# Kernel optimization log

Hardware: AMD Instinct MI355X
Metric: run time of the kernel (lower is better)

## Reference

```python
import jax, jax.numpy as jnp
import numpy as np

N, E, G = 20000, 100000, 32
HID, HEADS, HC = 64, 8, 64  # hidden, heads, per-head channels (PyG: out_channels per head)
L, K = 3, 4


def setup_inputs() -> dict:
    key = jax.random.key(0)
    ks = jax.random.split(key, 20)
    rn = lambda k, s, sc=0.05: jax.random.normal(k, s, jnp.float32) * sc
    HO = HEADS * HC  # 512
    return {
        "x": jax.random.uniform(ks[0], (N, 7), jnp.float32),
        "edge_attr": jax.random.normal(ks[1], (E, 4), jnp.float32),
        "means": jax.random.normal(ks[2], (K, 8), jnp.float32),
        "log_stds": jnp.zeros((K, 8), jnp.float32),
        "sp_W": rn(ks[3], (K, HID), 0.3), "sp_b": jnp.zeros((HID,), jnp.float32),
        "ne_W": rn(ks[4], (7, HID), 0.3), "ne_b": jnp.zeros((HID,), jnp.float32),
        "ee_W": rn(ks[5], (4, HID), 0.3), "ee_b": jnp.zeros((HID,), jnp.float32),
        "Wq": rn(ks[6], (L, HID, HO)), "bq": jnp.zeros((L, HO), jnp.float32),
        "Wk": rn(ks[7], (L, HID, HO)), "bk": jnp.zeros((L, HO), jnp.float32),
        "Wv": rn(ks[8], (L, HID, HO)), "bv": jnp.zeros((L, HO), jnp.float32),
        "We": rn(ks[9], (L, HID, HO)), "be": jnp.zeros((L, HO), jnp.float32),
        "Ws": rn(ks[10], (L, HID, HID)), "bs": jnp.zeros((L, HID), jnp.float32),
        "eu_W": rn(ks[11], (L, 3 * HID, HID)), "eu_b": jnp.zeros((L, HID), jnp.float32),
        "rW1": rn(ks[12], (2 * HID, HID)), "rb1": jnp.zeros((HID,), jnp.float32),
        "rW2": rn(ks[13], (HID, HID)), "rb2": jnp.zeros((HID,), jnp.float32),
        "rW3": rn(ks[14], (HID, 2)), "rb3": jnp.zeros((2,), jnp.float32),
        "edge_index": jax.random.randint(ks[15], (2, E), 0, N, jnp.int32),
        "batch": jnp.sort(jax.random.randint(ks[16], (N,), 0, G, jnp.int32)),
        "num_graphs": G,
    }


def reference(x, edge_attr, means, log_stds, sp_W, sp_b, ne_W, ne_b, ee_W, ee_b,
              Wq, bq, Wk, bk, Wv, bv, We, be, Ws, bs, eu_W, eu_b,
              rW1, rb1, rW2, rb2, rW3, rb3, edge_index, batch, num_graphs):
    n = x.shape[0]
    src, dst = edge_index[0], edge_index[1]

    # ---- SpatialGaussianEncoder (dropout is identity in eval) ----
    p = x[:, :4]
    sl, sr = p[src, :2], p[src, 2:4]
    dl, dr = p[dst, :2], p[dst, 2:4]
    rel = jnp.stack([dl - sl, dl - sr, dr - sl, dr - sr], axis=1)  # [E,4,2]
    dist = jnp.linalg.norm(rel, axis=-1)                           # [E,4]
    ang = jnp.arctan2(rel[..., 1], rel[..., 0])                    # [E,4]
    u = jnp.stack([dist, ang], axis=-1).reshape(-1, 8)             # [E,8] (d,a)x4
    std = jnp.exp(log_stds) + 1e-6                                 # [K,8]
    z = (u[:, None, :] - means[None]) / std[None]                  # [E,K,8]
    w = jnp.exp(-0.5 * jnp.sum(z * z, axis=-1))                    # [E,K]
    sp = jax.nn.relu(w @ sp_W + sp_b)                              # [E,HID]

    h = jax.nn.relu(x @ ne_W + ne_b)                               # [N,HID]
    ea = jax.nn.relu(edge_attr @ ee_W + ee_b) + sp                 # [E,HID]

    scale = 1.0 / float(np.sqrt(HC))
    for l in range(L):
        # PyG TransformerConv(hidden, hidden, heads=8, edge_dim=hidden, concat=False)
        q = (h @ Wq[l] + bq[l]).reshape(n, HEADS, HC)
        k = (h @ Wk[l] + bk[l]).reshape(n, HEADS, HC)
        v = (h @ Wv[l] + bv[l]).reshape(n, HEADS, HC)
        e = (ea @ We[l] + be[l]).reshape(-1, HEADS, HC)
        kj = k[src] + e                                            # [E,H,C]
        alpha = jnp.einsum('ehc,ehc->eh', q[dst], kj) * scale      # [E,H]
        m = jax.ops.segment_max(alpha, dst, num_segments=n)
        ex = jnp.exp(alpha - m[dst])
        den = jax.ops.segment_sum(ex, dst, num_segments=n)
        a = ex / (den[dst] + 1e-16)                                # scatter-softmax over dst
        msg = a[:, :, None] * (v[src] + e)                         # [E,H,C]
        out = jax.ops.segment_sum(msg, dst, num_segments=n).mean(axis=1)  # concat=False -> head mean
        h = jax.nn.relu(out + h @ Ws[l] + bs[l])                   # skip (root_weight) + F.relu
        ef = jnp.concatenate([h[src], h[dst], ea], axis=1)         # [E,3*HID]
        ea = jax.nn.relu(ef @ eu_W[l] + eu_b[l])

    # ---- per-graph masked-mean pooling == segment mean ----
    cn = jnp.maximum(jax.ops.segment_sum(jnp.ones((n,), x.dtype), batch, num_segments=num_graphs), 1.0)
    node_pool = jax.ops.segment_sum(h, batch, num_segments=num_graphs) / cn[:, None]
    eb = batch[src]
    ce = jnp.maximum(jax.ops.segment_sum(jnp.ones((src.shape[0],), x.dtype), eb, num_segments=num_graphs), 1.0)
    edge_pool = jax.ops.segment_sum(ea, eb, num_segments=num_graphs) / ce[:, None]
    g = jnp.concatenate([node_pool, edge_pool], axis=1)            # [G,2*HID]

    h1 = jax.nn.relu(g @ rW1 + rb1)
    h2 = jax.nn.relu(h1 @ rW2 + rb2)
    return jnp.tanh(h2 @ rW3 + rb3)                                # [G,2]
```

## Files before the change

### kernel.cpp

```cpp
#include <hip/hip_runtime.h>
#include <hip/hip_bf16.h>
#include <cstdint>
#include <cstddef>



__global__ void __launch_bounds__(256) k_node_embed(
    const float* __restrict__ x, const float* __restrict__ neW, const float* __restrict__ neb,
    float* __restrict__ h, int N)
{
    int idx = blockIdx.x * 256 + threadIdx.x;
    int n = idx >> 6, c = idx & 63;
    if (n >= N) return;
    float acc = neb[c];
    #pragma unroll
    for (int j = 0; j < 7; ++j) acc += x[(size_t)n * 7 + j] * neW[j * 64 + c];
    h[(size_t)n * 64 + c] = fmaxf(acc, 0.f);
}

__global__ void __launch_bounds__(256) k_edge_w(
    const float* __restrict__ x,
    const float* __restrict__ means, const float* __restrict__ log_stds,
    const int2* __restrict__ ipair, const int* __restrict__ idst,
    float* __restrict__ wbuf, int E)
{
    int slot = blockIdx.x * 256 + threadIdx.x;
    if (slot >= E) return;
    int s = ipair[slot].x, d = idst[slot];
    const float* ps = x + (size_t)s * 7;
    const float* pd = x + (size_t)d * 7;
    float slx = ps[0], sly = ps[1], srx = ps[2], sry = ps[3];
    float dlx = pd[0], dly = pd[1], drx = pd[2], dry = pd[3];
    float u[8];
    float rx, ry;
    rx = dlx - slx; ry = dly - sly; u[0] = sqrtf(rx*rx + ry*ry); u[1] = atan2f(ry, rx);
    rx = dlx - srx; ry = dly - sry; u[2] = sqrtf(rx*rx + ry*ry); u[3] = atan2f(ry, rx);
    rx = drx - slx; ry = dry - sly; u[4] = sqrtf(rx*rx + ry*ry); u[5] = atan2f(ry, rx);
    rx = drx - srx; ry = dry - sry; u[6] = sqrtf(rx*rx + ry*ry); u[7] = atan2f(ry, rx);
    #pragma unroll
    for (int kk = 0; kk < 4; ++kk) {
        float ssum = 0.f;
        #pragma unroll
        for (int dd = 0; dd < 8; ++dd) {
            float stdv = expf(log_stds[kk*8+dd]) + 1e-6f;
            float z = (u[dd] - means[kk*8+dd]) / stdv;
            ssum += z * z;
        }
        wbuf[(size_t)slot*4 + kk] = expf(-0.5f * ssum);
    }
}

__global__ void __launch_bounds__(256) k_edge_ea(
    const float* __restrict__ edge_attr, const float* __restrict__ wbuf,
    const int2* __restrict__ ipair,
    const float* __restrict__ spW, const float* __restrict__ spb,
    const float* __restrict__ eeW, const float* __restrict__ eeb,
    float* __restrict__ ea, int E)
{
    int idx = blockIdx.x * 256 + threadIdx.x;
    int slot = idx >> 6, c = idx & 63;
    if (slot >= E) return;
    int e = ipair[slot].y;
    float acce = eeb[c];
    #pragma unroll
    for (int j = 0; j < 4; ++j) acce += edge_attr[(size_t)e*4 + j] * eeW[j*64 + c];
    float accs = spb[c];
    #pragma unroll
    for (int j = 0; j < 4; ++j) accs += wbuf[(size_t)slot*4 + j] * spW[j*64 + c];
    ea[(size_t)slot*64 + c] = fmaxf(acce, 0.f) + fmaxf(accs, 0.f);
}


__global__ void __launch_bounds__(256) k_hist(
    const int* __restrict__ dst, int* __restrict__ deg, int E)
{
    int e = blockIdx.x * 256 + threadIdx.x;
    if (e < E) atomicAdd(deg + dst[e], 1);
}

__global__ void __launch_bounds__(1024) k_scan(
    const int* __restrict__ deg, int* __restrict__ ptr, int* __restrict__ headw, int N)
{
    __shared__ int part[1024];
    int t = threadIdx.x;
    int per = (N + 1023) / 1024;
    int s = 0;
    for (int i = 0; i < per; ++i) { int idx = t*per + i; if (idx < N) s += deg[idx]; }
    part[t] = s;
    __syncthreads();
    for (int off = 1; off < 1024; off <<= 1) {
        int v = (t >= off) ? part[t - off] : 0;
        __syncthreads();
        part[t] += v;
        __syncthreads();
    }
    int base = (t > 0) ? part[t - 1] : 0;
    for (int i = 0; i < per; ++i) {
        int idx = t*per + i;
        if (idx < N) { ptr[idx] = base; headw[idx] = base; base += deg[idx]; }
    }
    if (t == 1023) ptr[N] = part[1023];
}

__global__ void __launch_bounds__(256) k_scatter(
    const int* __restrict__ dst, const int* __restrict__ src, const int* __restrict__ batch,
    int* __restrict__ headw, int2* __restrict__ ipair, int* __restrict__ idst,
    int* __restrict__ iebs, int E)
{
    int e = blockIdx.x * 256 + threadIdx.x;
    if (e < E) {
        int s = src[e];
        int d = dst[e];
        int pos = atomicAdd(headw + d, 1);
        ipair[pos] = make_int2(s, e);
        idst[pos] = d;
        iebs[pos] = batch[s];
    }
}


__global__ void __launch_bounds__(256) k_wprod_all(
    const float* __restrict__ Wq, const float* __restrict__ bq,
    const float* __restrict__ Wk, const float* __restrict__ We,
    float* __restrict__ Mk, float* __restrict__ Me,
    float* __restrict__ bqk, float* __restrict__ bqe)
{
    int h = blockIdx.x;
    int which = blockIdx.y;
    int l = blockIdx.z;
    const float* Wq_l = Wq + (size_t)l * 64 * 512;
    const float* bq_l = bq + (size_t)l * 512;
    const float* Wx_l = (which ? We : Wk) + (size_t)l * 64 * 512;
    float* M  = (which ? Me : Mk) + (size_t)l * 64 * 512;
    float* bM = (which ? bqe : bqk) + (size_t)l * 512;
    __shared__ float wq_s[65][64];
    __shared__ float wx_s[64][65];
    int tid = threadIdx.x;
    for (int i = tid; i < 4096; i += 256) {
        int r = i >> 6, c2 = i & 63;
        wq_s[r][c2] = Wq_l[(size_t)r*512 + h*64 + c2];
        wx_s[r][c2] = Wx_l[(size_t)r*512 + h*64 + c2];
    }
    if (tid < 64) wq_s[64][tid] = bq_l[h*64 + tid];
    __syncthreads();
    int j = tid & 63, cg = tid >> 6;
    for (int c = cg*16; c < cg*16 + 16; ++c) {
        float s = 0.f;
        #pragma unroll 8
        for (int c2 = 0; c2 < 64; ++c2) s += wq_s[c][c2] * wx_s[j][c2];
        M[(size_t)c*512 + h*64 + j] = s;
    }
    if (tid < 64) {
        float s = 0.f;
        #pragma unroll 8
        for (int c2 = 0; c2 < 64; ++c2) s += wq_s[64][c2] * wx_s[tid][c2];
        bM[h*64 + tid] = s;
    }
}

__global__ void __launch_bounds__(64) k_wqb_all(
    const float* __restrict__ Wq, const float* __restrict__ bq,
    const float* __restrict__ bk, const float* __restrict__ be,
    float* __restrict__ wqb, float* __restrict__ cb)
{
    int l = blockIdx.x;
    const float* Wq_l = Wq + (size_t)l * 64 * 512;
    const float* bq_l = bq + (size_t)l * 512;
    const float* bk_l = bk + (size_t)l * 512;
    const float* be_l = be + (size_t)l * 512;
    float* wqb_l = wqb + (size_t)l * 512;
    float* cb_l  = cb + (size_t)l * 8;
    int c = threadIdx.x;
    for (int h = 0; h < 8; ++h) {
        float s = 0.f;
        for (int c2 = 0; c2 < 64; ++c2)
            s += Wq_l[(size_t)c*512 + h*64 + c2] * (bk_l[h*64+c2] + be_l[h*64+c2]);
        wqb_l[c*8 + h] = s;
    }
    if (c < 8) {
        float s = 0.f;
        for (int c2 = 0; c2 < 64; ++c2)
            s += bq_l[c*64 + c2] * (bk_l[c*64+c2] + be_l[c*64+c2]);
        cb_l[c] = s;
    }
}


__global__ void __launch_bounds__(256) k_proj16(
    const float* __restrict__ h,
    const float* __restrict__ Mk, const float* __restrict__ bqk, float* __restrict__ qk,
    const float* __restrict__ Me, const float* __restrict__ bqe, float* __restrict__ qe2,
    int N)
{
    __shared__ float As[64][132];
    __shared__ __align__(16) float Wt[64][64];
    int tid = threadIdx.x;
    int y = blockIdx.y;
    int which = y >> 3, yb = y & 7;
    const float* W    = which ? Me : Mk;
    const float* bias = (which ? bqe : bqk) + yb * 64;
    float* Y          = which ? qe2 : qk;
    int n0 = blockIdx.x * 128;
    {
        int rt = tid & 127;
        int n = n0 + rt;
        int jh = (tid >> 7) * 32;
        if (n < N) {
            const float* ap = h + (size_t)n*64;
            #pragma unroll
            for (int j4 = 0; j4 < 8; ++j4) {
                int j = jh + j4 * 4;
                float4 a = *(const float4*)(ap + j);
                As[j+0][rt] = a.x; As[j+1][rt] = a.y;
                As[j+2][rt] = a.z; As[j+3][rt] = a.w;
            }
        } else {
            #pragma unroll
            for (int j4 = 0; j4 < 8; ++j4) {
                int j = jh + j4 * 4;
                As[j+0][rt] = 0.f; As[j+1][rt] = 0.f;
                As[j+2][rt] = 0.f; As[j+3][rt] = 0.f;
            }
        }
        #pragma unroll
        for (int i = 0; i < 4; ++i) {
            int idx = tid + i * 256;
            int j = idx >> 4, c4 = (idx & 15) * 4;
            *(float4*)&Wt[j][c4] = *(const float4*)(W + (size_t)j*512 + yb*64 + c4);
        }
    }
    __syncthreads();
    int wv = tid >> 6, lane = tid & 63;
    int rg = lane >> 3, cg = lane & 7;
    int c0 = cg * 8;
    int rbase = wv * 32 + rg * 4;
    float acc[4][8];
    float4 b0 = *(const float4*)(bias + c0);
    float4 b1 = *(const float4*)(bias + c0 + 4);
    #pragma unroll
    for (int t = 0; t < 4; ++t) {
        acc[t][0]=b0.x; acc[t][1]=b0.y; acc[t][2]=b0.z; acc[t][3]=b0.w;
        acc[t][4]=b1.x; acc[t][5]=b1.y; acc[t][6]=b1.z; acc[t][7]=b1.w;
    }
    #pragma unroll 4
    for (int j = 0; j < 64; ++j) {
        float4 av = *(const float4*)&As[j][rbase];
        float4 w0 = *(const float4*)&Wt[j][c0];
        float4 w1 = *(const float4*)&Wt[j][c0 + 4];
        acc[0][0] += av.x*w0.x; acc[0][1] += av.x*w0.y; acc[0][2] += av.x*w0.z; acc[0][3] += av.x*w0.w;
        acc[0][4] += av.x*w1.x; acc[0][5] += av.x*w1.y; acc[0][6] += av.x*w1.z; acc[0][7] += av.x*w1.w;
        acc[1][0] += av.y*w0.x; acc[1][1] += av.y*w0.y; acc[1][2] += av.y*w0.z; acc[1][3] += av.y*w0.w;
        acc[1][4] += av.y*w1.x; acc[1][5] += av.y*w1.y; acc[1][6] += av.y*w1.z; acc[1][7] += av.y*w1.w;
        acc[2][0] += av.z*w0.x; acc[2][1] += av.z*w0.y; acc[2][2] += av.z*w0.z; acc[2][3] += av.z*w0.w;
        acc[2][4] += av.z*w1.x; acc[2][5] += av.z*w1.y; acc[2][6] += av.z*w1.z; acc[2][7] += av.z*w1.w;
        acc[3][0] += av.w*w0.x; acc[3][1] += av.w*w0.y; acc[3][2] += av.w*w0.z; acc[3][3] += av.w*w0.w;
        acc[3][4] += av.w*w1.x; acc[3][5] += av.w*w1.y; acc[3][6] += av.w*w1.z; acc[3][7] += av.w*w1.w;
    }
    #pragma unroll
    for (int t = 0; t < 4; ++t) {
        int n = n0 + rbase + t;
        if (n < N) {
            float4 o0 = {acc[t][0],acc[t][1],acc[t][2],acc[t][3]};
            float4 o1 = {acc[t][4],acc[t][5],acc[t][6],acc[t][7]};
            *(float4*)(Y + (size_t)n*512 + yb*64 + c0)     = o0;
            *(float4*)(Y + (size_t)n*512 + yb*64 + c0 + 4) = o1;
        }
    }
}


__global__ void __launch_bounds__(256) k_attn_fused(
    const float* __restrict__ qk, const float* __restrict__ qe2,
    const float* __restrict__ wqb, const float* __restrict__ cb,
    const float* __restrict__ ea, const float* __restrict__ hbuf,
    const int* __restrict__ ptr, const int2* __restrict__ ipair,
    float* __restrict__ hagg, float* __restrict__ tbuf, float* __restrict__ sbuf, int N)
{
    int wv = threadIdx.x >> 6, lane = threadIdx.x & 63;
    int n = blockIdx.x * 4 + wv;
    if (n >= N) return;
    int h = lane >> 3, p = lane & 7;
    int b = ptr[n], e_ = ptr[n + 1];
    int deg = e_ - b;
    const float4* xp = (const float4*)(qk + (size_t)n*512 + lane*8);
    float4 x0 = xp[0], x1 = xp[1];
    const float4* gp = (const float4*)(qe2 + (size_t)n*512 + lane*8);
    float4 g0 = gp[0], g1 = gp[1];
    const float4* hdp = (const float4*)(hbuf + (size_t)n*64 + p*8);
    float4 hd0 = hdp[0], hd1 = hdp[1];
    float qbh = hd0.x*wqb[(p*8+0)*8+h] + hd0.y*wqb[(p*8+1)*8+h]
              + hd0.z*wqb[(p*8+2)*8+h] + hd0.w*wqb[(p*8+3)*8+h]
              + hd1.x*wqb[(p*8+4)*8+h] + hd1.y*wqb[(p*8+5)*8+h]
              + hd1.z*wqb[(p*8+6)*8+h] + hd1.w*wqb[(p*8+7)*8+h];
    qbh += __shfl_xor(qbh, 1);
    qbh += __shfl_xor(qbh, 2);
    qbh += __shfl_xor(qbh, 4);
    qbh += cb[h];
    float m = -3.4e38f, den = 0.f;
    float hacc[8], tacc[8];
    #pragma unroll
    for (int i = 0; i < 8; ++i) { hacc[i] = 0.f; tacc[i] = 0.f; }
    for (int base = 0; base < deg; base += 64) {
        int cnt = deg - base; if (cnt > 64) cnt = 64;
        int2 myp = (lane < cnt) ? ipair[b + base + lane] : make_int2(0, 0);
        int s0i = __shfl(myp.x, 0);
        const float4* hp = (const float4*)(hbuf + (size_t)s0i*64 + p*8);
        const float4* ap = (const float4*)(ea + (size_t)(b + base)*64 + p*8);
        float4 h0 = hp[0], h1 = hp[1];
        float4 a0 = ap[0], a1 = ap[1];
        for (int i = 0; i < cnt; ++i) {
            float4 h0c = h0, h1c = h1, a0c = a0, a1c = a1;
            if (i + 1 < cnt) {
                int sn = __shfl(myp.x, i + 1);
                const float4* hpn = (const float4*)(hbuf + (size_t)sn*64 + p*8);
                const float4* apn = (const float4*)(ea + (size_t)(b + base + i + 1)*64 + p*8);
                h0 = hpn[0]; h1 = hpn[1]; a0 = apn[0]; a1 = apn[1];
            }
            float t = x0.x*h0c.x + x0.y*h0c.y + x0.z*h0c.z + x0.w*h0c.w
                    + x1.x*h1c.x + x1.y*h1c.y + x1.z*h1c.z + x1.w*h1c.w
                    + g0.x*a0c.x + g0.y*a0c.y + g0.z*a0c.z + g0.w*a0c.w
                    + g1.x*a1c.x + g1.y*a1c.y + g1.z*a1c.z + g1.w*a1c.w;
            t += __shfl_xor(t, 1);
            t += __shfl_xor(t, 2);
            t += __shfl_xor(t, 4);
            float al = 0.125f * (t + qbh);
            float mn = fmaxf(m, al);
            float r = expf(m - mn);
            float w = expf(al - mn);
            den = den * r + w;
            m = mn;
            hacc[0] = hacc[0]*r + w*h0c.x; hacc[1] = hacc[1]*r + w*h0c.y;
            hacc[2] = hacc[2]*r + w*h0c.z; hacc[3] = hacc[3]*r + w*h0c.w;
            hacc[4] = hacc[4]*r + w*h1c.x; hacc[5] = hacc[5]*r + w*h1c.y;
            hacc[6] = hacc[6]*r + w*h1c.z; hacc[7] = hacc[7]*r + w*h1c.w;
            tacc[0] = tacc[0]*r + w*a0c.x; tacc[1] = tacc[1]*r + w*a0c.y;
            tacc[2] = tacc[2]*r + w*a0c.z; tacc[3] = tacc[3]*r + w*a0c.w;
            tacc[4] = tacc[4]*r + w*a1c.x; tacc[5] = tacc[5]*r + w*a1c.y;
            tacc[6] = tacc[6]*r + w*a1c.z; tacc[7] = tacc[7]*r + w*a1c.w;
        }
    }
    float inv = 0.125f / (den + 1e-16f);
    float4 o;
    o = {hacc[0]*inv,hacc[1]*inv,hacc[2]*inv,hacc[3]*inv};
    *(float4*)(hagg + (size_t)n*512 + lane*8)     = o;
    o = {hacc[4]*inv,hacc[5]*inv,hacc[6]*inv,hacc[7]*inv};
    *(float4*)(hagg + (size_t)n*512 + lane*8 + 4) = o;
    o = {tacc[0]*inv,tacc[1]*inv,tacc[2]*inv,tacc[3]*inv};
    *(float4*)(tbuf + (size_t)n*512 + lane*8)     = o;
    o = {tacc[4]*inv,tacc[5]*inv,tacc[6]*inv,tacc[7]*inv};
    *(float4*)(tbuf + (size_t)n*512 + lane*8 + 4) = o;
    if (p == 0) sbuf[(size_t)n*8 + h] = den * inv;
}

__global__ void __launch_bounds__(256) k_nf_gemm2(
    const float* __restrict__ tbuf, const float* __restrict__ hagg,
    const float* __restrict__ We, const float* __restrict__ Wv,
    float* __restrict__ pbuf, int N)
{
    __shared__ float As[64][132];
    __shared__ __align__(16) float Wt[64][64];
    int tid = threadIdx.x;
    int y = blockIdx.y;
    int n0 = blockIdx.x * 128;
    int wv = tid >> 6, lane = tid & 63;
    int rg = lane >> 3, cg = lane & 7;
    int c0 = cg * 8;
    int rbase = wv * 32 + rg * 4;
    float acc[4][8];
    #pragma unroll
    for (int t = 0; t < 4; ++t)
        #pragma unroll
        for (int i = 0; i < 8; ++i) acc[t][i] = 0.f;
    #pragma unroll
    for (int round = 0; round < 2; ++round) {
        const float* A = round ? hagg : tbuf;
        const float* W = round ? Wv : We;
        if (round) __syncthreads();
        {
            int rt = tid & 127;
            int n = n0 + rt;
            int jh = (tid >> 7) * 32;
            if (n < N) {
                const float* ap = A + (size_t)n*512 + y*64;
                #pragma unroll
                for (int j4 = 0; j4 < 8; ++j4) {
                    int j = jh + j4 * 4;
                    float4 a = *(const float4*)(ap + j);
                    As[j+0][rt] = a.x; As[j+1][rt] = a.y;
                    As[j+2][rt] = a.z; As[j+3][rt] = a.w;
                }
            } else {
                #pragma unroll
                for (int j4 = 0; j4 < 8; ++j4) {
                    int j = jh + j4 * 4;
                    As[j+0][rt] = 0.f; As[j+1][rt] = 0.f;
                    As[j+2][rt] = 0.f; As[j+3][rt] = 0.f;
                }
            }
            #pragma unroll
            for (int i = 0; i < 4; ++i) {
                int idx = tid + i * 256;
                int j = idx >> 4, c4 = (idx & 15) * 4;
                *(float4*)&Wt[j][c4] = *(const float4*)(W + (size_t)j*512 + y*64 + c4);
            }
        }
        __syncthreads();
        #pragma unroll 4
        for (int j = 0; j < 64; ++j) {
            float4 av = *(const float4*)&As[j][rbase];
            float4 w0 = *(const float4*)&Wt[j][c0];
            float4 w1 = *(const float4*)&Wt[j][c0 + 4];
            acc[0][0] += av.x*w0.x; acc[0][1] += av.x*w0.y; acc[0][2] += av.x*w0.z; acc[0][3] += av.x*w0.w;
            acc[0][4] += av.x*w1.x; acc[0][5] += av.x*w1.y; acc[0][6] += av.x*w1.z; acc[0][7] += av.x*w1.w;
            acc[1][0] += av.y*w0.x; acc[1][1] += av.y*w0.y; acc[1][2] += av.y*w0.z; acc[1][3] += av.y*w0.w;
            acc[1][4] += av.y*w1.x; acc[1][5] += av.y*w1.y; acc[1][6] += av.y*w1.z; acc[1][7] += av.y*w1.w;
            acc[2][0] += av.z*w0.x; acc[2][1] += av.z*w0.y; acc[2][2] += av.z*w0.z; acc[2][3] += av.z*w0.w;
            acc[2][4] += av.z*w1.x; acc[2][5] += av.z*w1.y; acc[2][6] += av.z*w1.z; acc[2][7] += av.z*w1.w;
            acc[3][0] += av.w*w0.x; acc[3][1] += av.w*w0.y; acc[3][2] += av.w*w0.z; acc[3][3] += av.w*w0.w;
            acc[3][4] += av.w*w1.x; acc[3][5] += av.w*w1.y; acc[3][6] += av.w*w1.z; acc[3][7] += av.w*w1.w;
        }
    }
    float* out = pbuf + (size_t)y * N * 64;
    #pragma unroll
    for (int t = 0; t < 4; ++t) {
        int n = n0 + rbase + t;
        if (n < N) {
            float4 o0 = {acc[t][0],acc[t][1],acc[t][2],acc[t][3]};
            float4 o1 = {acc[t][4],acc[t][5],acc[t][6],acc[t][7]};
            *(float4*)(out + (size_t)n*64 + c0)     = o0;
            *(float4*)(out + (size_t)n*64 + c0 + 4) = o1;
        }
    }
}

__global__ void __launch_bounds__(256) k_nf_reduce2(
    const float* __restrict__ pbuf, const float* __restrict__ hin,
    const float* __restrict__ sbuf, const float* __restrict__ Ws,
    const float* __restrict__ be, const float* __restrict__ bv,
    const float* __restrict__ bs, float* __restrict__ hnext, int N)
{
    int idx = blockIdx.x * 256 + threadIdx.x;
    int n = idx >> 6, cc = idx & 63;
    if (n >= N) return;
    float a = bs[cc];
    #pragma unroll
    for (int y = 0; y < 8; ++y) a += pbuf[(size_t)y*N*64 + (size_t)n*64 + cc];
    float hv = hin[(size_t)n*64 + cc];
    #pragma unroll 8
    for (int j = 0; j < 64; ++j) a += __shfl(hv, j) * Ws[(size_t)j*64 + cc];
    #pragma unroll
    for (int h = 0; h < 8; ++h)
        a += sbuf[(size_t)n*8 + h] * (be[h*64 + cc] + bv[h*64 + cc]);
    hnext[(size_t)n*64 + cc] = fmaxf(a, 0.f);
}

__global__ void __launch_bounds__(256) k_eu_pre(
    const float* __restrict__ h, const float* __restrict__ euW,
    float* __restrict__ hw, int N)
{
    __shared__ float As[64][132];
    __shared__ __align__(16) float Wt[64][64];
    int tid = threadIdx.x;
    int y = blockIdx.y;
    int n0 = blockIdx.x * 128;
    {
        int rt = tid & 127;
        int n = n0 + rt;
        int jh = (tid >> 7) * 32;
        if (n < N) {
            const float* ap = h + (size_t)n*64;
            #pragma unroll
            for (int j4 = 0; j4 < 8; ++j4) {
                int j = jh + j4 * 4;
                float4 a = *(const float4*)(ap + j);
                As[j+0][rt] = a.x; As[j+1][rt] = a.y;
                As[j+2][rt] = a.z; As[j+3][rt] = a.w;
            }
        } else {
            #pragma unroll
            for (int j4 = 0; j4 < 8; ++j4) {
                int j = jh + j4 * 4;
                As[j+0][rt] = 0.f; As[j+1][rt] = 0.f;
                As[j+2][rt] = 0.f; As[j+3][rt] = 0.f;
            }
        }
        #pragma unroll
        for (int i = 0; i < 4; ++i) {
            int idx = tid + i * 256;
            *(float4*)&Wt[idx >> 4][(idx & 15) * 4] =
                *(const float4*)(euW + (size_t)y*4096 + idx * 4);
        }
    }
    __syncthreads();
    int wv = tid >> 6, lane = tid & 63;
    int rg = lane >> 3, cg = lane & 7;
    int c0 = cg * 8;
    int rbase = wv * 32 + rg * 4;
    float acc[4][8];
    #pragma unroll
    for (int t = 0; t < 4; ++t)
        #pragma unroll
        for (int i = 0; i < 8; ++i) acc[t][i] = 0.f;
    #pragma unroll 4
    for (int j = 0; j < 64; ++j) {
        float4 av = *(const float4*)&As[j][rbase];
        float4 w0 = *(const float4*)&Wt[j][c0];
        float4 w1 = *(const float4*)&Wt[j][c0 + 4];
        acc[0][0] += av.x*w0.x; acc[0][1] += av.x*w0.y; acc[0][2] += av.x*w0.z; acc[0][3] += av.x*w0.w;
        acc[0][4] += av.x*w1.x; acc[0][5] += av.x*w1.y; acc[0][6] += av.x*w1.z; acc[0][7] += av.x*w1.w;
        acc[1][0] += av.y*w0.x; acc[1][1] += av.y*w0.y; acc[1][2] += av.y*w0.z; acc[1][3] += av.y*w0.w;
        acc[1][4] += av.y*w1.x; acc[1][5] += av.y*w1.y; acc[1][6] += av.y*w1.z; acc[1][7] += av.y*w1.w;
        acc[2][0] += av.z*w0.x; acc[2][1] += av.z*w0.y; acc[2][2] += av.z*w0.z; acc[2][3] += av.z*w0.w;
        acc[2][4] += av.z*w1.x; acc[2][5] += av.z*w1.y; acc[2][6] += av.z*w1.z; acc[2][7] += av.z*w1.w;
        acc[3][0] += av.w*w0.x; acc[3][1] += av.w*w0.y; acc[3][2] += av.w*w0.z; acc[3][3] += av.w*w0.w;
        acc[3][4] += av.w*w1.x; acc[3][5] += av.w*w1.y; acc[3][6] += av.w*w1.z; acc[3][7] += av.w*w1.w;
    }
    #pragma unroll
    for (int t = 0; t < 4; ++t) {
        int n = n0 + rbase + t;
        if (n < N) {
            float4 o0 = {acc[t][0],acc[t][1],acc[t][2],acc[t][3]};
            float4 o1 = {acc[t][4],acc[t][5],acc[t][6],acc[t][7]};
            *(float4*)(hw + (size_t)n*128 + y*64 + c0)     = o0;
            *(float4*)(hw + (size_t)n*128 + y*64 + c0 + 4) = o1;
        }
    }
}

__global__ void __launch_bounds__(256) k_edge_update2(
    const float* __restrict__ hw, const float* __restrict__ ea,
    const float* __restrict__ euW2, const float* __restrict__ eub,
    const int2* __restrict__ ipair, const int* __restrict__ idst,
    float* __restrict__ ea2, int E)
{
    __shared__ float As[64][132];
    __shared__ __align__(16) float Wt[64][64];
    __shared__ int sid[128], did[128];
    int tid = threadIdx.x;
    int e0 = blockIdx.x * 128;
    if (tid < 128) {
        int slot = e0 + tid; if (slot >= E) slot = E - 1;
        sid[tid] = ipair[slot].x; did[tid] = idst[slot];
    }
    {
        int et = tid & 127;
        int slot = e0 + et; if (slot >= E) slot = E - 1;
        const float* ap = ea + (size_t)slot * 64;
        int jh = (tid >> 7) * 32;
        #pragma unroll
        for (int j4 = 0; j4 < 8; ++j4) {
            int j = jh + j4 * 4;
            float4 a = *(const float4*)(ap + j);
            As[j+0][et] = a.x; As[j+1][et] = a.y;
            As[j+2][et] = a.z; As[j+3][et] = a.w;
        }
        #pragma unroll
        for (int i = 0; i < 4; ++i) {
            int idx = tid + i * 256;
            *(float4*)&Wt[idx >> 4][(idx & 15) * 4] = *(const float4*)(euW2 + idx * 4);
        }
    }
    __syncthreads();
    int wv = tid >> 6, lane = tid & 63;
    int rg = lane >> 3, cg = lane & 7;
    int c0 = cg * 8;
    int rbase = wv * 32 + rg * 4;
    float acc[4][8];
    float4 b0 = *(const float4*)(eub + c0);
    float4 b1 = *(const float4*)(eub + c0 + 4);
    #pragma unroll
    for (int t = 0; t < 4; ++t) {
        acc[t][0]=b0.x; acc[t][1]=b0.y; acc[t][2]=b0.z; acc[t][3]=b0.w;
        acc[t][4]=b1.x; acc[t][5]=b1.y; acc[t][6]=b1.z; acc[t][7]=b1.w;
    }
    #pragma unroll 4
    for (int j = 0; j < 64; ++j) {
        float4 av = *(const float4*)&As[j][rbase];
        float4 w0 = *(const float4*)&Wt[j][c0];
        float4 w1 = *(const float4*)&Wt[j][c0 + 4];
        acc[0][0] += av.x*w0.x; acc[0][1] += av.x*w0.y; acc[0][2] += av.x*w0.z; acc[0][3] += av.x*w0.w;
        acc[0][4] += av.x*w1.x; acc[0][5] += av.x*w1.y; acc[0][6] += av.x*w1.z; acc[0][7] += av.x*w1.w;
        acc[1][0] += av.y*w0.x; acc[1][1] += av.y*w0.y; acc[1][2] += av.y*w0.z; acc[1][3] += av.y*w0.w;
        acc[1][4] += av.y*w1.x; acc[1][5] += av.y*w1.y; acc[1][6] += av.y*w1.z; acc[1][7] += av.y*w1.w;
        acc[2][0] += av.z*w0.x; acc[2][1] += av.z*w0.y; acc[2][2] += av.z*w0.z; acc[2][3] += av.z*w0.w;
        acc[2][4] += av.z*w1.x; acc[2][5] += av.z*w1.y; acc[2][6] += av.z*w1.z; acc[2][7] += av.z*w1.w;
        acc[3][0] += av.w*w0.x; acc[3][1] += av.w*w0.y; acc[3][2] += av.w*w0.z; acc[3][3] += av.w*w0.w;
        acc[3][4] += av.w*w1.x; acc[3][5] += av.w*w1.y; acc[3][6] += av.w*w1.z; acc[3][7] += av.w*w1.w;
    }
    #pragma unroll
    for (int t = 0; t < 4; ++t) {
        int slot = e0 + rbase + t;
        if (slot < E) {
            int s = sid[rbase + t], d = did[rbase + t];
            const float4* sp = (const float4*)(hw + (size_t)s*128 + c0);
            const float4* dp = (const float4*)(hw + (size_t)d*128 + 64 + c0);
            float4 s0 = sp[0], s1 = sp[1];
            float4 d0 = dp[0], d1 = dp[1];
            float4 o0 = {fmaxf(acc[t][0]+s0.x+d0.x,0.f), fmaxf(acc[t][1]+s0.y+d0.y,0.f),
                         fmaxf(acc[t][2]+s0.z+d0.z,0.f), fmaxf(acc[t][3]+s0.w+d0.w,0.f)};
            float4 o1 = {fmaxf(acc[t][4]+s1.x+d1.x,0.f), fmaxf(acc[t][5]+s1.y+d1.y,0.f),
                         fmaxf(acc[t][6]+s1.z+d1.z,0.f), fmaxf(acc[t][7]+s1.w+d1.w,0.f)};
            *(float4*)(ea2 + (size_t)slot*64 + c0)     = o0;
            *(float4*)(ea2 + (size_t)slot*64 + c0 + 4) = o1;
        }
    }
}


__global__ void __launch_bounds__(64) k_node_pool(
    const float* __restrict__ h, const int* __restrict__ batch,
    float* __restrict__ npool, float* __restrict__ cn, int N)
{
    int lane = threadIdx.x;
    int n0 = blockIdx.x * 64;
    float acc = 0.f; int cur = -1; int run = 0;
    for (int i = 0; i < 64; ++i) {
        int n = n0 + i;
        if (n >= N) break;
        int b = batch[n];
        if (b != cur) {
            if (cur >= 0) {
                atomicAdd(npool + (size_t)cur*64 + lane, acc);
                if (lane == 0) atomicAdd(cn + cur, (float)run);
            }
            cur = b; acc = 0.f; run = 0;
        }
        acc += h[(size_t)n*64 + lane];
        ++run;
    }
    if (cur >= 0) {
        atomicAdd(npool + (size_t)cur*64 + lane, acc);
        if (lane == 0) atomicAdd(cn + cur, (float)run);
    }
}

__global__ void __launch_bounds__(256) k_edge_pool2(
    const float* __restrict__ ea, const int* __restrict__ iebs,
    float* __restrict__ rep, int E)
{
    __shared__ float pool_s[32][64];
    __shared__ float cnt_s[32];
    int tid = threadIdx.x;
    for (int i = tid; i < 2048; i += 256) ((float*)pool_s)[i] = 0.f;
    if (tid < 32) cnt_s[tid] = 0.f;
    __syncthreads();
    int wv = tid >> 6, lane = tid & 63;
    int base = blockIdx.x * 64 + wv * 16;
    int b16[16]; float v16[16];
    #pragma unroll
    for (int u = 0; u < 16; ++u) {
        int slot = base + u;
        bool ok = (slot < E);
        b16[u] = ok ? iebs[slot] : -1;
        v16[u] = ok ? ea[(size_t)slot*64 + lane] : 0.f;
    }
    #pragma unroll
    for (int u = 0; u < 16; ++u) {
        if (b16[u] >= 0) {
            atomicAdd(&pool_s[b16[u]][lane], v16[u]);
            if (lane == 0) atomicAdd(&cnt_s[b16[u]], 1.f);
        }
    }
    __syncthreads();
    float* myrep = rep + (size_t)(blockIdx.x & 7) * 2080;
    for (int i = tid; i < 2048; i += 256) atomicAdd(myrep + i, ((float*)pool_s)[i]);
    if (tid < 32) atomicAdd(myrep + 2048 + tid, cnt_s[tid]);
}

__global__ void __launch_bounds__(256) k_pool_merge(
    const float* __restrict__ rep, float* __restrict__ epool, float* __restrict__ ce)
{
    int i = blockIdx.x * 256 + threadIdx.x;
    if (i < 2080) {
        float s = 0.f;
        #pragma unroll
        for (int r = 0; r < 8; ++r) s += rep[(size_t)r*2080 + i];
        if (i < 2048) epool[i] = s; else ce[i - 2048] = s;
    }
}

__global__ void __launch_bounds__(64) k_head_mlp(
    const float* __restrict__ npool, const float* __restrict__ epool,
    const float* __restrict__ cn, const float* __restrict__ ce,
    const float* __restrict__ rW1, const float* __restrict__ rb1,
    const float* __restrict__ rW2, const float* __restrict__ rb2,
    const float* __restrict__ rW3, const float* __restrict__ rb3,
    float* __restrict__ out)
{
    __shared__ float g[128];
    __shared__ float h1[64];
    __shared__ float h2[64];
    int b = blockIdx.x, lane = threadIdx.x;
    float cnv = fmaxf(cn[b], 1.f), cev = fmaxf(ce[b], 1.f);
    g[lane]      = npool[(size_t)b*64 + lane] / cnv;
    g[64 + lane] = epool[(size_t)b*64 + lane] / cev;
    __syncthreads();
    float acc = rb1[lane];
    #pragma unroll 4
    for (int j = 0; j < 128; ++j) acc += g[j] * rW1[j*64 + lane];
    h1[lane] = fmaxf(acc, 0.f);
    __syncthreads();
    acc = rb2[lane];
    #pragma unroll 4
    for (int j = 0; j < 64; ++j) acc += h1[j] * rW2[j*64 + lane];
    h2[lane] = fmaxf(acc, 0.f);
    __syncthreads();
    if (lane < 2) {
        float o = rb3[lane];
        for (int j = 0; j < 64; ++j) o += h2[j] * rW3[j*2 + lane];
        out[b*2 + lane] = tanhf(o);
    }
}


extern "C" void kernel_launch(void* const* d_in, const int* in_sizes, int n_in,
                              void* d_out, int out_size, void* d_ws, size_t ws_size,
                              hipStream_t stream)
{
    const float* x         = (const float*)d_in[0];
    const float* edge_attr = (const float*)d_in[1];
    const float* means     = (const float*)d_in[2];
    const float* log_stds  = (const float*)d_in[3];
    const float* spW       = (const float*)d_in[4];
    const float* spb       = (const float*)d_in[5];
    const float* neW       = (const float*)d_in[6];
    const float* neb       = (const float*)d_in[7];
    const float* eeW       = (const float*)d_in[8];
    const float* eeb       = (const float*)d_in[9];
    const float* Wq        = (const float*)d_in[10];
    const float* bq        = (const float*)d_in[11];
    const float* Wk        = (const float*)d_in[12];
    const float* bk        = (const float*)d_in[13];
    const float* Wv        = (const float*)d_in[14];
    const float* bv        = (const float*)d_in[15];
    const float* We        = (const float*)d_in[16];
    const float* be        = (const float*)d_in[17];
    const float* Ws        = (const float*)d_in[18];
    const float* bs        = (const float*)d_in[19];
    const float* euW       = (const float*)d_in[20];
    const float* eub       = (const float*)d_in[21];
    const float* rW1       = (const float*)d_in[22];
    const float* rb1       = (const float*)d_in[23];
    const float* rW2       = (const float*)d_in[24];
    const float* rb2       = (const float*)d_in[25];
    const float* rW3       = (const float*)d_in[26];
    const float* rb3       = (const float*)d_in[27];
    const int* eidx        = (const int*)d_in[28];
    const int* batch       = (const int*)d_in[29];

    int N = in_sizes[0] / 7;
    int E = in_sizes[1] / 4;
    const int G = 32;
    const int* srcp = eidx;
    const int* dstp = eidx + E;

    float* ws = (float*)d_ws;
    size_t fl = 0;
    float* hA    = ws + fl; fl += (size_t)N * 64;
    float* hB    = ws + fl; fl += (size_t)N * 64;
    float* eaA   = ws + fl; fl += (size_t)E * 64;
    float* eaB   = ws + fl; fl += (size_t)E * 64;
    float* B1    = ws + fl; fl += (size_t)N * 512;
    float* B2    = ws + fl; fl += (size_t)N * 512;
    float* B3    = ws + fl; fl += (size_t)N * 512;
    float* alpha = ws + fl; fl += (size_t)E * 8;
    float* sbuf  = ws + fl; fl += (size_t)N * 8;
    float* npool = ws + fl; fl += (size_t)G * 64;
    float* epool = ws + fl; fl += (size_t)G * 64;
    float* cn    = ws + fl; fl += G;
    float* ce    = ws + fl; fl += G;
    float* Mk3   = ws + fl; fl += 3 * 64 * 512;
    float* Me3   = ws + fl; fl += 3 * 64 * 512;
    float* bqk3  = ws + fl; fl += 3 * 512;
    float* bqe3  = ws + fl; fl += 3 * 512;
    float* wqb3  = ws + fl; fl += 3 * 512;
    float* cb3   = ws + fl; fl += 24;
    float* rep   = ws + fl; fl += 8 * 2080;
    int* ideg  = (int*)(ws + fl); fl += (size_t)N;
    int* ihead = (int*)(ws + fl); fl += (size_t)N;
    int2* ipair = (int2*)(ws + fl); fl += (size_t)E * 2;
    int* idst  = (int*)(ws + fl); fl += (size_t)E;
    int* iebs  = (int*)(ws + fl); fl += (size_t)E;
    int* iptr  = (int*)(ws + fl); fl += (size_t)N + 1;

    float* wbuf = alpha;

    hipMemsetAsync(npool, 0, (size_t)(G * 130) * sizeof(float), stream);
    hipMemsetAsync(rep, 0, (size_t)(8 * 2080) * sizeof(float), stream);
    hipMemsetAsync(ideg, 0, (size_t)N * sizeof(int), stream);

    k_node_embed<<<(N * 64 + 255) / 256, 256, 0, stream>>>(x, neW, neb, hA, N);
    k_hist<<<(E + 255) / 256, 256, 0, stream>>>(dstp, ideg, E);
    k_scan<<<1, 1024, 0, stream>>>(ideg, iptr, ihead, N);
    k_scatter<<<(E + 255) / 256, 256, 0, stream>>>(dstp, srcp, batch, ihead,
                                                   ipair, idst, iebs, E);
    k_edge_w<<<(E + 255) / 256, 256, 0, stream>>>(x, means, log_stds, ipair, idst, wbuf, E);
    k_edge_ea<<<((size_t)E * 64 + 255) / 256, 256, 0, stream>>>(edge_attr, wbuf, ipair,
                                                                spW, spb, eeW, eeb, eaA, E);
    k_wprod_all<<<dim3(8, 2, 3), 256, 0, stream>>>(Wq, bq, Wk, We, Mk3, Me3, bqk3, bqe3);
    k_wqb_all<<<3, 64, 0, stream>>>(Wq, bq, bk, be, wqb3, cb3);

    float* hcur = hA;  float* hnext = hB;
    float* eacur = eaA; float* eanext = eaB;
    for (int l = 0; l < 3; ++l) {
        const float* Wv_l = Wv + (size_t)l * 64 * 512;
        const float* We_l = We + (size_t)l * 64 * 512;
        const float* bv_l = bv + (size_t)l * 512;
        const float* be_l = be + (size_t)l * 512;
        const float* euW_l = euW + (size_t)l * 192 * 64;

        k_proj16<<<dim3((N + 127) / 128, 16), 256, 0, stream>>>(
            hcur,
            Mk3 + (size_t)l * 32768, bqk3 + (size_t)l * 512, B1,
            Me3 + (size_t)l * 32768, bqe3 + (size_t)l * 512, B2, N);

        k_attn_fused<<<(N + 3) / 4, 256, 0, stream>>>(B1, B2,
                                                      wqb3 + (size_t)l * 512,
                                                      cb3 + (size_t)l * 8,
                                                      eacur, hcur,
                                                      iptr, ipair,
                                                      B1 , B2 , sbuf, N);
        k_nf_gemm2<<<dim3((N + 127) / 128, 8), 256, 0, stream>>>(B2, B1, We_l, Wv_l, B3, N);
        k_nf_reduce2<<<((size_t)N * 64 + 255) / 256, 256, 0, stream>>>(B3, hcur, sbuf,
                                                                       Ws + (size_t)l * 64 * 64,
                                                                       be_l, bv_l,
                                                                       bs + (size_t)l * 64,
                                                                       hnext, N);
        k_eu_pre<<<dim3((N + 127) / 128, 2), 256, 0, stream>>>(hnext, euW_l, B3, N);
        k_edge_update2<<<(E + 127) / 128, 256, 0, stream>>>(B3, eacur, euW_l + 2 * 4096,
                                                            eub + (size_t)l * 64,
                                                            ipair, idst, eanext, E);
        float* t1 = hcur; hcur = hnext; hnext = t1;
        float* t2 = eacur; eacur = eanext; eanext = t2;
    }

    k_node_pool<<<(N + 63) / 64, 64, 0, stream>>>(hcur, batch, npool, cn, N);
    k_edge_pool2<<<(E + 63) / 64, 256, 0, stream>>>(eacur, iebs, rep, E);
    k_pool_merge<<<9, 256, 0, stream>>>(rep, epool, ce);
    k_head_mlp<<<G, 64, 0, stream>>>(npool, epool, cn, ce, rW1, rb1, rW2, rb2, rW3, rb3,
                                     (float*)d_out);
}
```

Before: 716.8 us.

## Process attention nodes in descending-degree order via degree counting sort

Adds three small kernels that histogram node in-degrees, scan them in descending order, and build a permutation of nodes sorted by degree. The fused attention kernel then assigns each wavefront a node from that permutation, so the four wavefronts in a block have similar edge counts and high-degree nodes start first. The aim is to reduce load imbalance and tail effects from the degree distribution. In exchange there are three extra launches plus a memset, and node accesses to q/k buffers become non-sequential, which can hurt memory locality.

```diff
diff --git a/kernel.cpp b/kernel.cpp
--- a/kernel.cpp
+++ b/kernel.cpp
@@ -115,6 +115,39 @@
         ipair[pos] = make_int2(s, e);
         idst[pos] = d;
         iebs[pos] = batch[s];
+    }
+}
+
+
+__global__ void __launch_bounds__(256) k_dhist(
+    const int* __restrict__ ptr, int* __restrict__ dcnt, int N)
+{
+    int n = blockIdx.x * 256 + threadIdx.x;
+    if (n < N) {
+        int dg = ptr[n + 1] - ptr[n];
+        if (dg > 255) dg = 255;
+        atomicAdd(dcnt + dg, 1);
+    }
+}
+
+__global__ void __launch_bounds__(256) k_dscan(
+    const int* __restrict__ dcnt, int* __restrict__ dhead)
+{
+    int b = threadIdx.x;
+    int s = 0;
+    for (int b2 = b + 1; b2 < 256; ++b2) s += dcnt[b2];
+    dhead[b] = s;
+}
+
+__global__ void __launch_bounds__(256) k_dscatter(
+    const int* __restrict__ ptr, int* __restrict__ dhead, int* __restrict__ nperm, int N)
+{
+    int n = blockIdx.x * 256 + threadIdx.x;
+    if (n < N) {
+        int dg = ptr[n + 1] - ptr[n];
+        if (dg > 255) dg = 255;
+        int pos = atomicAdd(dhead + dg, 1);
+        nperm[pos] = n;
     }
 }
 
@@ -274,11 +307,13 @@
     const float* __restrict__ wqb, const float* __restrict__ cb,
     const float* __restrict__ ea, const float* __restrict__ hbuf,
     const int* __restrict__ ptr, const int2* __restrict__ ipair,
+    const int* __restrict__ nperm,
     float* __restrict__ hagg, float* __restrict__ tbuf, float* __restrict__ sbuf, int N)
 {
     int wv = threadIdx.x >> 6, lane = threadIdx.x & 63;
-    int n = blockIdx.x * 4 + wv;
-    if (n >= N) return;
+    int idx = blockIdx.x * 4 + wv;
+    if (idx >= N) return;
+    int n = nperm[idx];
     int h = lane >> 3, p = lane & 7;
     int b = ptr[n], e_ = ptr[n + 1];
     int deg = e_ - b;
@@ -782,18 +817,25 @@
     int* idst  = (int*)(ws + fl); fl += (size_t)E;
     int* iebs  = (int*)(ws + fl); fl += (size_t)E;
     int* iptr  = (int*)(ws + fl); fl += (size_t)N + 1;
+    int* nperm = (int*)(ws + fl); fl += (size_t)N;
+    int* dcnt  = (int*)(ws + fl); fl += 256;
+    int* dhead = (int*)(ws + fl); fl += 256;
 
     float* wbuf = alpha;
 
     hipMemsetAsync(npool, 0, (size_t)(G * 130) * sizeof(float), stream);
     hipMemsetAsync(rep, 0, (size_t)(8 * 2080) * sizeof(float), stream);
     hipMemsetAsync(ideg, 0, (size_t)N * sizeof(int), stream);
+    hipMemsetAsync(dcnt, 0, 256 * sizeof(int), stream);
 
     k_node_embed<<<(N * 64 + 255) / 256, 256, 0, stream>>>(x, neW, neb, hA, N);
     k_hist<<<(E + 255) / 256, 256, 0, stream>>>(dstp, ideg, E);
     k_scan<<<1, 1024, 0, stream>>>(ideg, iptr, ihead, N);
     k_scatter<<<(E + 255) / 256, 256, 0, stream>>>(dstp, srcp, batch, ihead,
                                                    ipair, idst, iebs, E);
+    k_dhist<<<(N + 255) / 256, 256, 0, stream>>>(iptr, dcnt, N);
+    k_dscan<<<1, 256, 0, stream>>>(dcnt, dhead);
+    k_dscatter<<<(N + 255) / 256, 256, 0, stream>>>(iptr, dhead, nperm, N);
     k_edge_w<<<(E + 255) / 256, 256, 0, stream>>>(x, means, log_stds, ipair, idst, wbuf, E);
     k_edge_ea<<<((size_t)E * 64 + 255) / 256, 256, 0, stream>>>(edge_attr, wbuf, ipair,
                                                                 spW, spb, eeW, eeb, eaA, E);
@@ -818,7 +860,7 @@
                                                       wqb3 + (size_t)l * 512,
                                                       cb3 + (size_t)l * 8,
                                                       eacur, hcur,
-                                                      iptr, ipair,
+                                                      iptr, ipair, nperm,
                                                       B1 , B2 , sbuf, N);
         k_nf_gemm2<<<dim3((N + 127) / 128, 8), 256, 0, stream>>>(B2, B1, We_l, Wv_l, B3, N);
         k_nf_reduce2<<<((size_t)N * 64 + 255) / 256, 256, 0, stream>>>(B3, hcur, sbuf,
```

Result: slower. 878.3 us (+22.5%).
